# Performance work log

Measured on AMD Instinct MI355X. Metric: run time of the kernel, lower is better.

The kernel has to match this reference:

```python
import jax, jax.numpy as jnp
import numpy as np

WIN = (2, 7, 7)
SHIFT = (1, 3, 3)
HEADS = 4
DIM = 128
MLP_HID = 512
N = WIN[0] * WIN[1] * WIN[2]  # 98
EPS = 1e-5


def _rel_pos_index():
    d = np.arange(WIN[0]); h = np.arange(WIN[1]); w = np.arange(WIN[2])
    coords = np.stack(np.meshgrid(d, h, w, indexing='ij'))  # (3, Wd, Wh, Ww)
    flat = coords.reshape(3, -1)  # (3, N)
    rel = flat[:, :, None] - flat[:, None, :]  # (3, N, N)
    rel = rel.transpose(1, 2, 0).astype(np.int64)  # (N, N, 3)
    rel[..., 0] += WIN[0] - 1
    rel[..., 1] += WIN[1] - 1
    rel[..., 2] += WIN[2] - 1
    rel[..., 0] *= (2 * WIN[1] - 1) * (2 * WIN[2] - 1)
    rel[..., 1] *= (2 * WIN[2] - 1)
    return rel.sum(-1)  # (N, N)


def setup_inputs() -> dict:
    key = jax.random.key(0)
    ks = jax.random.split(key, 8)
    B, D, H, W, C = 4, 8, 56, 56, DIM
    tbl_size = (2 * WIN[0] - 1) * (2 * WIN[1] - 1) * (2 * WIN[2] - 1)  # 507
    s = 0.02
    return {
        'x': jax.random.normal(ks[0], (B, D, H, W, C), jnp.float32),
        'rel_idx': jnp.asarray(_rel_pos_index(), jnp.int32),
        'rpb_table': s * jax.random.normal(ks[1], (tbl_size, HEADS), jnp.float32),
        'qkv_w': s * jax.random.normal(ks[2], (C, 3 * C), jnp.float32),
        'qkv_b': jnp.zeros((3 * C,), jnp.float32),
        'proj_w': s * jax.random.normal(ks[3], (C, C), jnp.float32),
        'proj_b': jnp.zeros((C,), jnp.float32),
        'ln1_g': jnp.ones((C,), jnp.float32),
        'ln1_b': jnp.zeros((C,), jnp.float32),
        'ln2_g': jnp.ones((C,), jnp.float32),
        'ln2_b': jnp.zeros((C,), jnp.float32),
        'mlp_w1': s * jax.random.normal(ks[4], (C, MLP_HID), jnp.float32),
        'mlp_b1': jnp.zeros((MLP_HID,), jnp.float32),
        'mlp_w2': s * jax.random.normal(ks[5], (MLP_HID, C), jnp.float32),
        'mlp_b2': jnp.zeros((C,), jnp.float32),
    }


def _layernorm(x, g, b):
    mu = jnp.mean(x, -1, keepdims=True)
    var = jnp.var(x, -1, keepdims=True)
    return (x - mu) * jax.lax.rsqrt(var + EPS) * g + b


def _window_partition(x):
    B, Dp, Hp, Wp, C = x.shape
    x = x.reshape(B, Dp // WIN[0], WIN[0], Hp // WIN[1], WIN[1], Wp // WIN[2], WIN[2], C)
    x = x.transpose(0, 1, 3, 5, 2, 4, 6, 7)
    return x.reshape(-1, N, C)


def _window_reverse(win, B, Dp, Hp, Wp):
    C = win.shape[-1]
    x = win.reshape(B, Dp // WIN[0], Hp // WIN[1], Wp // WIN[2], WIN[0], WIN[1], WIN[2], C)
    x = x.transpose(0, 1, 4, 2, 5, 3, 6, 7)
    return x.reshape(B, Dp, Hp, Wp, C)


def _block(x, rel_idx, rpb_table, qkv_w, qkv_b, proj_w, proj_b,
           ln1_g, ln1_b, ln2_g, ln2_b, mlp_w1, mlp_b1, mlp_w2, mlp_b2):
    B, D, H, W, C = x.shape
    shortcut = x
    x = _layernorm(x, ln1_g, ln1_b)
    pad_d = (-D) % WIN[0]; pad_h = (-H) % WIN[1]; pad_w = (-W) % WIN[2]
    x = jnp.pad(x, ((0, 0), (0, pad_d), (0, pad_h), (0, pad_w), (0, 0)))
    _, Dp, Hp, Wp, _ = x.shape
    x = jnp.roll(x, (-SHIFT[0], -SHIFT[1], -SHIFT[2]), axis=(1, 2, 3))
    xw = _window_partition(x)  # (B_, N, C)
    B_ = xw.shape[0]
    hd = C // HEADS
    qkv = (xw @ qkv_w + qkv_b).reshape(B_, N, 3, HEADS, hd).transpose(2, 0, 3, 1, 4)
    q, k, v = qkv[0], qkv[1], qkv[2]  # (B_, h, N, hd)
    q = q * (hd ** -0.5)
    attn = jnp.einsum('bhnd,bhmd->bhnm', q, k)
    bias = rpb_table[rel_idx.reshape(-1)].reshape(N, N, HEADS).transpose(2, 0, 1)
    attn = attn + bias[None]
    # NOTE: the original module calls attn with mask=None even when shifted.
    attn = jax.nn.softmax(attn, axis=-1)
    out = jnp.einsum('bhnm,bhmd->bhnd', attn, v).transpose(0, 2, 1, 3).reshape(B_, N, C)
    out = out @ proj_w + proj_b
    x = _window_reverse(out, B, Dp, Hp, Wp)
    x = jnp.roll(x, (SHIFT[0], SHIFT[1], SHIFT[2]), axis=(1, 2, 3))
    x = x[:, :D, :H, :W, :]
    x = shortcut + x
    h1 = _layernorm(x, ln2_g, ln2_b)
    h1 = jax.nn.gelu(h1 @ mlp_w1 + mlp_b1, approximate=False)
    return x + (h1 @ mlp_w2 + mlp_b2)


def reference(x, rel_idx, rpb_table, qkv_w, qkv_b, proj_w, proj_b,
              ln1_g, ln1_b, ln2_g, ln2_b, mlp_w1, mlp_b1, mlp_w2, mlp_b2):
    return _block(x, rel_idx, rpb_table, qkv_w, qkv_b, proj_w, proj_b,
                  ln1_g, ln1_b, ln2_g, ln2_b, mlp_w1, mlp_b1, mlp_w2, mlp_b2)
```

## Files before the change

kernel.cpp:

```cpp
#include <hip/hip_runtime.h>
#include <hip/hip_bf16.h>
#include <cstdint>

#define NWIN   1024
#define NTOK   98
#define BIAS_N 9604

typedef __attribute__((ext_vector_type(8))) short bf16x8;
typedef __attribute__((ext_vector_type(4))) float f32x4;

__device__ __forceinline__ float b2f(unsigned short u) {
  union { uint32_t i; float f; } v; v.i = ((uint32_t)u) << 16; return v.f;
}
__device__ __forceinline__ float b2f_lo(uint32_t u) {
  union { uint32_t i; float f; } v; v.i = u << 16; return v.f;
}
__device__ __forceinline__ float b2f_hi(uint32_t u) {
  union { uint32_t i; float f; } v; v.i = u & 0xffff0000u; return v.f;
}
__device__ __forceinline__ unsigned short f2b(float f) {
  union { float f; uint32_t i; } v; v.f = f;
  uint32_t r = v.i + 0x7fffu + ((v.i >> 16) & 1u);
  return (unsigned short)(r >> 16);
}
__device__ __forceinline__ float ldf(const void* p, size_t i, int f32) {
  return f32 ? ((const float*)p)[i] : b2f(((const unsigned short*)p)[i]);
}
__device__ __forceinline__ float2 ldf2(const void* p, size_t i, int f32) {
  if (f32) { const float* q = (const float*)p + i; return make_float2(q[0], q[1]); }
  uint32_t u = *(const uint32_t*)((const unsigned short*)p + i);
  return make_float2(b2f_lo(u), b2f_hi(u));
}
__device__ __forceinline__ int detect_f32(const uint32_t* __restrict__ xw, int lane) {
  uint32_t w = xw[lane];
  int e = (w >> 23) & 0xFF;
  unsigned long long m = __ballot(e >= 112 && e <= 134);
  return __popcll(m) >= 32;
}
__device__ __forceinline__ float gelu_f(float x) {
  float a = fabsf(x) * 0.70710678118654752f;
  float t = __builtin_amdgcn_rcpf(1.0f + 0.3275911f * a);
  float p = ((((1.061405429f * t - 1.453152027f) * t + 1.421413741f) * t
              - 0.284496736f) * t + 0.254829592f) * t;
  float erfp = 1.0f - p * __expf(-a * a);
  return 0.5f * x * (1.0f + copysignf(erfp, x));
}

#define QG_OFF   0
#define KG_OFF   25690112
#define VGT_OFF  51380224
#define ZPAD_OFF 80740352
#define BIAS_OFF 80748544
#define WQ_OFF   80902208
#define WP_OFF   81000512
#define W1_OFF   81033280
#define W2_OFF   81164352
#define PAR_OFF  81295424
#define FLAG_OFF 81302080
#define LNG_OFF  81302144
#define P_LN1G 0
#define P_LN1B 128
#define P_LN2G 256
#define P_LN2B 384
#define P_QKVB 512
#define P_PROJB 896
#define P_B1  1024
#define P_B2  1536

__global__ __launch_bounds__(256) void prep_kernel(
    const uint32_t* __restrict__ xw,
    const void* __restrict__ qkvw, const void* __restrict__ projw,
    const void* __restrict__ w1, const void* __restrict__ w2,
    const void* __restrict__ ln1g, const void* __restrict__ ln1b,
    const void* __restrict__ ln2g, const void* __restrict__ ln2b,
    const void* __restrict__ qkvb, const void* __restrict__ projb,
    const void* __restrict__ b1, const void* __restrict__ b2,
    const int* __restrict__ rel_idx, const void* __restrict__ tbl,
    unsigned short* __restrict__ wq_t, unsigned short* __restrict__ wp_t,
    unsigned short* __restrict__ w1_t, unsigned short* __restrict__ w2_t,
    float* __restrict__ par, unsigned short* __restrict__ zpad,
    float* __restrict__ bias) {
  const int f32 = detect_f32(xw, threadIdx.x & 63);
  const int bid = blockIdx.x;
  if (bid < 791) {
    int idx = bid * 256 + threadIdx.x;
    if (idx < 49152) {
      int n = idx >> 7, k = idx & 127;
      wq_t[idx] = f2b(ldf(qkvw, (size_t)k * 384 + n, f32));
    } else if ((idx -= 49152) < 16384) {
      int n = idx >> 7, k = idx & 127;
      wp_t[idx] = f2b(ldf(projw, (size_t)k * 128 + n, f32));
    } else if ((idx -= 16384) < 65536) {
      int n = idx >> 7, k = idx & 127;
      w1_t[idx] = f2b(ldf(w1, (size_t)k * 512 + n, f32));
    } else if ((idx -= 65536) < 65536) {
      int n = idx >> 9, k = idx & 511;
      w2_t[idx] = f2b(ldf(w2, (size_t)k * 128 + n, f32));
    } else if ((idx -= 65536) < 1664) {
      float v;
      if      (idx < 128)  v = ldf(ln1g, idx, f32);
      else if (idx < 256)  v = ldf(ln1b, idx - 128, f32);
      else if (idx < 384)  v = ldf(ln2g, idx - 256, f32);
      else if (idx < 512)  v = ldf(ln2b, idx - 384, f32);
      else if (idx < 896)  v = ldf(qkvb, idx - 512, f32);
      else if (idx < 1024) v = ldf(projb, idx - 896, f32);
      else if (idx < 1536) v = ldf(b1, idx - 1024, f32);
      else                 v = ldf(b2, idx - 1536, f32);
      par[idx] = v;
    } else if ((idx -= 1664) < 4096) {
      zpad[idx] = 0;
    }
  } else {
    int i = (bid - 791) * 256 + threadIdx.x;
    if (i < 4 * BIAS_N) {
      int h = i / BIAS_N, ij = i % BIAS_N;
      bias[i] = ldf(tbl, (size_t)rel_idx[ij] * 4 + h, f32);
    }
  }
}

__global__ __launch_bounds__(256, 3) void attn_fused_kernel(
    const void* __restrict__ x,
    const unsigned short* __restrict__ wq_t, const float* __restrict__ bias,
    const unsigned short* __restrict__ wp_t, const float* __restrict__ par,
    unsigned short* __restrict__ kg, unsigned short* __restrict__ vgt,
    unsigned short* __restrict__ lng, void* __restrict__ out) {
  __shared__ __align__(16) unsigned short smem[25872];
  const int f32 = detect_f32((const uint32_t*)x, threadIdx.x & 63);
  const int tid = threadIdx.x, wave = tid >> 6, lane = tid & 63;
  const int quad = lane >> 4, lcol = lane & 15;
  const int win = blockIdx.x, h = wave;
  const int bb = win >> 8, rW = win & 255;
  const int wd = rW >> 6, r2 = rW & 63, wh = r2 >> 3, ww = r2 & 7;

  unsigned short* lnx = smem;
  unsigned short* qs  = smem + 13328;

  for (int t = wave; t < NTOK; t += 4) {
    int td = t / 49, r3 = t % 49, th = r3 / 7, tw = r3 % 7;
    int sd = (wd * 2 + td + 1) & 7;
    int sh = (wh * 7 + th + 3) % 56;
    int sw = (ww * 7 + tw + 3) % 56;
    size_t src = ((((size_t)bb * 8 + sd) * 56 + sh) * 56 + sw) * 128;
    int c0 = lane * 2;
    float2 f = ldf2(x, src + c0, f32);
    float s = f.x + f.y, ss = f.x * f.x + f.y * f.y;
#pragma unroll
    for (int off = 32; off >= 1; off >>= 1) { s += __shfl_xor(s, off); ss += __shfl_xor(ss, off); }
    float mu = s * (1.0f / 128.0f);
    float var = ss * (1.0f / 128.0f) - mu * mu;
    float rs = rsqrtf(var + 1e-5f);
    float y0 = (f.x - mu) * rs * par[P_LN1G + c0] + par[P_LN1B + c0];
    float y1 = (f.y - mu) * rs * par[P_LN1G + c0 + 1] + par[P_LN1B + c0 + 1];
    *(uint32_t*)(lnx + t * 136 + c0) = (uint32_t)f2b(y0) | ((uint32_t)f2b(y1) << 16);
  }
  __syncthreads();

  for (int p = 0; p < 6; ++p) {
    const int n = p * 64 + wave * 16 + lcol;
    bf16x8 bfr[4];
#pragma unroll
    for (int ks4 = 0; ks4 < 4; ++ks4)
      bfr[ks4] = *(const bf16x8*)(wq_t + (size_t)n * 128 + ks4 * 32 + quad * 8);
    const int region = p >> 1;
    const int head = (p & 1) * 2 + (wave >> 1);
    const int d = (wave & 1) * 16 + lcol;
    const float bc = par[P_QKVB + n];
    if (region == 0) {
      unsigned short* dstl = qs + head * 3136 + d;
      for (int mt = 0; mt < 7; ++mt) {
        f32x4 acc = (f32x4){0.f, 0.f, 0.f, 0.f};
#pragma unroll
        for (int ks4 = 0; ks4 < 4; ++ks4) {
          bf16x8 a = *(const bf16x8*)(lnx + min(mt * 16 + lcol, NTOK - 1) * 136 +
                                      ks4 * 32 + quad * 8);
          acc = __builtin_amdgcn_mfma_f32_16x16x32_bf16(a, bfr[ks4], acc, 0, 0, 0);
        }
#pragma unroll
        for (int rr = 0; rr < 4; ++rr) {
          int m = mt * 16 + quad * 4 + rr;
          if (m < NTOK) dstl[m * 32] = f2b((acc[rr] + bc) * 0.17677669529663687f);
        }
      }
    } else if (region == 1) {
      unsigned short* dstg = kg + ((size_t)win * 4 + head) * 3136 + d;
      for (int mt = 0; mt < 7; ++mt) {
        f32x4 acc = (f32x4){0.f, 0.f, 0.f, 0.f};
#pragma unroll
        for (int ks4 = 0; ks4 < 4; ++ks4) {
          bf16x8 a = *(const bf16x8*)(lnx + min(mt * 16 + lcol, NTOK - 1) * 136 +
                                      ks4 * 32 + quad * 8);
          acc = __builtin_amdgcn_mfma_f32_16x16x32_bf16(a, bfr[ks4], acc, 0, 0, 0);
        }
#pragma unroll
        for (int rr = 0; rr < 4; ++rr) {
          int m = mt * 16 + quad * 4 + rr;
          if (m < NTOK) dstg[m * 32] = f2b(acc[rr] + bc);
        }
      }
    } else {
      unsigned short* dstv = vgt + (((size_t)win * 4 + head) * 32 + d) * 112;
      for (int mt = 0; mt < 7; ++mt) {
        f32x4 acc = (f32x4){0.f, 0.f, 0.f, 0.f};
#pragma unroll
        for (int ks4 = 0; ks4 < 4; ++ks4) {
          bf16x8 a = *(const bf16x8*)(lnx + min(mt * 16 + lcol, NTOK - 1) * 136 +
                                      ks4 * 32 + quad * 8);
          acc = __builtin_amdgcn_mfma_f32_16x16x32_bf16(a, bfr[ks4], acc, 0, 0, 0);
        }
        ushort4 w;
        int m0 = mt * 16 + quad * 4;
        w.x = (m0 + 0 < NTOK) ? f2b(acc[0] + bc) : (unsigned short)0;
        w.y = (m0 + 1 < NTOK) ? f2b(acc[1] + bc) : (unsigned short)0;
        w.z = (m0 + 2 < NTOK) ? f2b(acc[2] + bc) : (unsigned short)0;
        w.w = (m0 + 3 < NTOK) ? f2b(acc[3] + bc) : (unsigned short)0;
        *(ushort4*)(dstv + m0) = w;
      }
    }
  }
  __syncthreads();

  const size_t hb = ((size_t)win * 4 + h) * 3136;
  const unsigned short* vbase = vgt + (((size_t)win * 4 + h) * 32) * 112;
  unsigned short* plh = smem + h * 2112;

  bf16x8 aq[7], bk[7];
#pragma unroll
  for (int t = 0; t < 7; ++t) {
    int row = min(t * 16 + lcol, NTOK - 1);
    aq[t] = *(const bf16x8*)(qs + h * 3136 + row * 32 + quad * 8);
    bk[t] = *(const bf16x8*)(kg + hb + (size_t)row * 32 + quad * 8);
  }
  for (int idx = lane; idx < 16 * 16; idx += 64) {
    int rr = idx >> 4, c = 112 + (idx & 15);
    plh[rr * 132 + c] = 0;
  }

  const float* bh = bias + h * BIAS_N;
  f32x4 o[7][2];
  for (int mt = 0; mt < 7; ++mt) {
    f32x4 s[7];
#pragma unroll
    for (int nt = 0; nt < 7; ++nt)
      s[nt] = __builtin_amdgcn_mfma_f32_16x16x32_bf16(aq[mt], bk[nt],
                                                      (f32x4){0.f, 0.f, 0.f, 0.f}, 0, 0, 0);
    const int ib = mt * 16 + quad * 4;
#pragma unroll
    for (int nt = 0; nt < 7; ++nt) {
      int j = nt * 16 + lcol;
      bool jv = j < NTOK;
#pragma unroll
      for (int r = 0; r < 4; ++r) {
        int ic = min(ib + r, NTOK - 1);
        s[nt][r] = jv ? (s[nt][r] + bh[ic * NTOK + j]) : -3.0e38f;
      }
    }
    float mx[4], sum[4], inv[4];
#pragma unroll
    for (int r = 0; r < 4; ++r) {
      float m = s[0][r];
#pragma unroll
      for (int nt = 1; nt < 7; ++nt) m = fmaxf(m, s[nt][r]);
      mx[r] = m;
    }
#pragma unroll
    for (int off = 1; off < 16; off <<= 1)
#pragma unroll
      for (int r = 0; r < 4; ++r) mx[r] = fmaxf(mx[r], __shfl_xor(mx[r], off));
#pragma unroll
    for (int r = 0; r < 4; ++r) sum[r] = 0.f;
#pragma unroll
    for (int nt = 0; nt < 7; ++nt)
#pragma unroll
      for (int r = 0; r < 4; ++r) {
        float e = __expf(s[nt][r] - mx[r]);
        s[nt][r] = e; sum[r] += e;
      }
#pragma unroll
    for (int off = 1; off < 16; off <<= 1)
#pragma unroll
      for (int r = 0; r < 4; ++r) sum[r] += __shfl_xor(sum[r], off);
#pragma unroll
    for (int r = 0; r < 4; ++r) inv[r] = 1.0f / sum[r];
#pragma unroll
    for (int nt = 0; nt < 7; ++nt)
#pragma unroll
      for (int r = 0; r < 4; ++r)
        plh[(quad * 4 + r) * 132 + nt * 16 + lcol] = f2b(s[nt][r] * inv[r]);
#pragma unroll
    for (int n2 = 0; n2 < 2; ++n2) {
      f32x4 acc = (f32x4){0.f, 0.f, 0.f, 0.f};
#pragma unroll
      for (int kp = 0; kp < 4; ++kp) {
        bf16x8 a = *(const bf16x8*)(plh + lcol * 132 + kp * 32 + quad * 8);
        bf16x8 b = *(const bf16x8*)(vbase + (size_t)(n2 * 16 + lcol) * 112 +
                                    kp * 32 + quad * 8);
        acc = __builtin_amdgcn_mfma_f32_16x16x32_bf16(a, b, acc, 0, 0, 0);
      }
      o[mt][n2] = acc;
    }
  }
  __syncthreads();

  unsigned short* olds = smem;
#pragma unroll
  for (int mt = 0; mt < 7; ++mt)
#pragma unroll
    for (int n2 = 0; n2 < 2; ++n2)
#pragma unroll
      for (int r = 0; r < 4; ++r)
        olds[(mt * 16 + quad * 4 + r) * 136 + h * 32 + n2 * 16 + lcol] = f2b(o[mt][n2][r]);
  __syncthreads();

  f32x4 pr[2][7];
  for (int t2 = 0; t2 < 2; ++t2) {
    const int n = (h * 2 + t2) * 16 + lcol;
    bf16x8 bw[4];
#pragma unroll
    for (int kp = 0; kp < 4; ++kp)
      bw[kp] = *(const bf16x8*)(wp_t + (size_t)n * 128 + kp * 32 + quad * 8);
    for (int mt = 0; mt < 7; ++mt) {
      f32x4 acc = (f32x4){0.f, 0.f, 0.f, 0.f};
#pragma unroll
      for (int kp = 0; kp < 4; ++kp) {
        bf16x8 a = *(const bf16x8*)(olds + (mt * 16 + lcol) * 136 + kp * 32 + quad * 8);
        acc = __builtin_amdgcn_mfma_f32_16x16x32_bf16(a, bw[kp], acc, 0, 0, 0);
      }
      pr[t2][mt] = acc;
    }
  }
  __syncthreads();

  const int c = (tid & 31) * 4;
  const float4 gv = *(const float4*)(par + P_LN2G + c);
  const float4 bv = *(const float4*)(par + P_LN2B + c);
  float* pout = (float*)smem;
  for (int pass = 0; pass < 2; ++pass) {
    const int mlo = pass * 56;
    for (int t2 = 0; t2 < 2; ++t2) {
      const int n = (h * 2 + t2) * 16 + lcol;
      const float bc = par[P_PROJB + n];
#pragma unroll
      for (int mt = 0; mt < 7; ++mt)
#pragma unroll
        for (int r = 0; r < 4; ++r) {
          int m = mt * 16 + quad * 4 + r;
          if (m >= mlo && m < mlo + 56 && m < NTOK)
            pout[(m - mlo) * 132 + n] = pr[t2][mt][r] + bc;
        }
    }
    __syncthreads();
    for (int i = tid >> 5; i < 56; i += 8) {
      int m = mlo + i;
      if (m >= NTOK) break;
      int td = m / 49, r3 = m % 49, th = r3 / 7, tw = r3 % 7;
      int sd = (wd * 2 + td + 1) & 7;
      int sh = (wh * 7 + th + 3) % 56;
      int sw = (ww * 7 + tw + 3) % 56;
      size_t base = ((((size_t)bb * 8 + sd) * 56 + sh) * 56 + sw) * 128 + c;
      float4 p = *(const float4*)(pout + i * 132 + c);
      float4 v;
      if (f32) {
        const float4 xr = *(const float4*)((const float*)x + base);
        v = make_float4(p.x + xr.x, p.y + xr.y, p.z + xr.z, p.w + xr.w);
        *(float4*)((float*)out + base) = v;
      } else {
        const ushort4 xr = *(const ushort4*)((const unsigned short*)x + base);
        v = make_float4(p.x + b2f(xr.x), p.y + b2f(xr.y),
                        p.z + b2f(xr.z), p.w + b2f(xr.w));
        ushort4 ov;
        ov.x = f2b(v.x); ov.y = f2b(v.y); ov.z = f2b(v.z); ov.w = f2b(v.w);
        *(ushort4*)((unsigned short*)out + base) = ov;
      }
      float s = v.x + v.y + v.z + v.w;
      float ss = v.x * v.x + v.y * v.y + v.z * v.z + v.w * v.w;
#pragma unroll
      for (int off = 1; off < 32; off <<= 1) {
        s += __shfl_xor(s, off); ss += __shfl_xor(ss, off);
      }
      float mu = s * (1.0f / 128.0f);
      float var = ss * (1.0f / 128.0f) - mu * mu;
      float rs = rsqrtf(var + 1e-5f);
      ushort4 lv;
      lv.x = f2b((v.x - mu) * rs * gv.x + bv.x);
      lv.y = f2b((v.y - mu) * rs * gv.y + bv.y);
      lv.z = f2b((v.z - mu) * rs * gv.z + bv.z);
      lv.w = f2b((v.w - mu) * rs * gv.w + bv.w);
      *(ushort4*)(lng + base) = lv;
    }
    if (pass == 0) __syncthreads();
  }
}

__global__ __launch_bounds__(256) void mlp_kernel(
    const unsigned short* __restrict__ w1_t, const unsigned short* __restrict__ w2_t,
    const float* __restrict__ par, const void* __restrict__ x,
    const unsigned short* __restrict__ lng, void* __restrict__ out) {
  __shared__ __align__(16) unsigned short hbuf[64 * 264];
  const int f32 = detect_f32((const uint32_t*)x, threadIdx.x & 63);
  const int tid = threadIdx.x, wave = tid >> 6, lane = tid & 63;
  const int quad = lane >> 4, lcol = lane & 15;
  const int m0 = blockIdx.x * 64;
  const int nb = wave * 16 + lcol;

  bf16x8 a1[4][4];
#pragma unroll
  for (int mt = 0; mt < 4; ++mt)
#pragma unroll
    for (int ks = 0; ks < 4; ++ks)
      a1[mt][ks] = *(const bf16x8*)(lng + (size_t)(m0 + mt * 16 + lcol) * 128 +
                                    ks * 32 + quad * 8);

  f32x4 acc2[2][4];
#pragma unroll
  for (int a = 0; a < 2; ++a)
#pragma unroll
    for (int b = 0; b < 4; ++b) acc2[a][b] = (f32x4){0.f, 0.f, 0.f, 0.f};

#pragma unroll 1
  for (int g = 0; g < 2; ++g) {
    for (int p = 0; p < 4; ++p) {
      const int nl = p * 64 + nb;
      const int n = g * 256 + nl;
      bf16x8 bfr[4];
#pragma unroll
      for (int ks = 0; ks < 4; ++ks)
        bfr[ks] = *(const bf16x8*)(w1_t + (size_t)n * 128 + ks * 32 + quad * 8);
      const float bc = par[P_B1 + n];
#pragma unroll
      for (int mt = 0; mt < 4; ++mt) {
        f32x4 acc = (f32x4){0.f, 0.f, 0.f, 0.f};
#pragma unroll
        for (int ks = 0; ks < 4; ++ks)
          acc = __builtin_amdgcn_mfma_f32_16x16x32_bf16(a1[mt][ks], bfr[ks], acc, 0, 0, 0);
#pragma unroll
        for (int rr = 0; rr < 4; ++rr) {
          int m = mt * 16 + quad * 4 + rr;
          hbuf[m * 264 + nl] = f2b(gelu_f(acc[rr] + bc));
        }
      }
    }
    __syncthreads();

#pragma unroll
    for (int np = 0; np < 2; ++np) {
      for (int kp = 0; kp < 2; ++kp) {
        bf16x8 b2r[4];
#pragma unroll
        for (int ks = 0; ks < 4; ++ks)
          b2r[ks] = *(const bf16x8*)(w2_t + (size_t)(np * 64 + nb) * 512 + g * 256 +
                                     kp * 128 + ks * 32 + quad * 8);
#pragma unroll
        for (int mt = 0; mt < 4; ++mt) {
#pragma unroll
          for (int ks = 0; ks < 4; ++ks) {
            bf16x8 a = *(const bf16x8*)(hbuf + (mt * 16 + lcol) * 264 + kp * 128 +
                                        ks * 32 + quad * 8);
            acc2[np][mt] = __builtin_amdgcn_mfma_f32_16x16x32_bf16(a, b2r[ks], acc2[np][mt], 0, 0, 0);
          }
        }
      }
    }
    __syncthreads();
  }

  float* pout = (float*)hbuf;
#pragma unroll
  for (int np = 0; np < 2; ++np) {
    const int n = np * 64 + nb;
    const float bc = par[P_B2 + n];
#pragma unroll
    for (int mt = 0; mt < 4; ++mt)
#pragma unroll
      for (int rr = 0; rr < 4; ++rr)
        pout[(mt * 16 + quad * 4 + rr) * 132 + n] = acc2[np][mt][rr] + bc;
  }
  __syncthreads();

  for (int i = tid; i < 2048; i += 256) {
    int t = i >> 5, c = (i & 31) * 4;
    size_t base = (size_t)(m0 + t) * 128 + c;
    float4 p = *(const float4*)(pout + t * 132 + c);
    if (f32) {
      const float4 xr = *(const float4*)((const float*)out + base);
      float4 ov = make_float4(p.x + xr.x, p.y + xr.y, p.z + xr.z, p.w + xr.w);
      *(float4*)((float*)out + base) = ov;
    } else {
      const ushort4 xr = *(const ushort4*)((const unsigned short*)out + base);
      ushort4 ov;
      ov.x = f2b(p.x + b2f(xr.x)); ov.y = f2b(p.y + b2f(xr.y));
      ov.z = f2b(p.z + b2f(xr.z)); ov.w = f2b(p.w + b2f(xr.w));
      *(ushort4*)((unsigned short*)out + base) = ov;
    }
  }
}

extern "C" void kernel_launch(void* const* d_in, const int* in_sizes, int n_in,
                              void* d_out, int out_size, void* d_ws, size_t ws_size,
                              hipStream_t stream) {
  const void* x      = d_in[0];
  const int*  rel    = (const int*)d_in[1];
  const void* rpb    = d_in[2];
  const void* qkv_w  = d_in[3];
  const void* qkv_b  = d_in[4];
  const void* proj_w = d_in[5];
  const void* proj_b = d_in[6];
  const void* ln1_g  = d_in[7];
  const void* ln1_b  = d_in[8];
  const void* ln2_g  = d_in[9];
  const void* ln2_b  = d_in[10];
  const void* w1     = d_in[11];
  const void* b1     = d_in[12];
  const void* w2     = d_in[13];
  const void* b2     = d_in[14];

  char* ws = (char*)d_ws;
  unsigned short* kg   = (unsigned short*)(ws + KG_OFF);
  unsigned short* vgt  = (unsigned short*)(ws + VGT_OFF);
  unsigned short* zpad = (unsigned short*)(ws + ZPAD_OFF);
  float*          bias = (float*)(ws + BIAS_OFF);
  unsigned short* wq_t = (unsigned short*)(ws + WQ_OFF);
  unsigned short* wp_t = (unsigned short*)(ws + WP_OFF);
  unsigned short* w1_t = (unsigned short*)(ws + W1_OFF);
  unsigned short* w2_t = (unsigned short*)(ws + W2_OFF);
  float*          par  = (float*)(ws + PAR_OFF);
  unsigned short* lng  = (unsigned short*)(ws + LNG_OFF);

  prep_kernel<<<791 + 151, 256, 0, stream>>>(
      (const uint32_t*)x, qkv_w, proj_w, w1, w2, ln1_g, ln1_b, ln2_g, ln2_b,
      qkv_b, proj_b, b1, b2, rel, rpb,
      wq_t, wp_t, w1_t, w2_t, par, zpad, bias);
  attn_fused_kernel<<<NWIN, 256, 0, stream>>>(x, wq_t, bias, wp_t, par,
                                              kg, vgt, lng, d_out);
  mlp_kernel<<<100352 / 64, 256, 0, stream>>>(w1_t, w2_t, par, x, lng, d_out);
}
```

Baseline: 364.0 us.

## Transpose and pad bias table, give each wave its own head's QKV, drop barrier

The relative-position bias is now precomputed transposed and zero-padded to 112x112 per head, so each lane loads four consecutive bias values with one float4 load instead of four scalar gathers. The QKV projection is remapped so each wave computes the Q, K and V columns of its own head. That removes the block-wide barrier between the projection and attention phases, leaving only a per-wave wait on outstanding memory ops. The P scratch buffer now reuses that wave's own Q region in shared memory instead of a separate slice. The risk is correctness: any later phase that still assumes cross-wave visibility could race, and the larger bias table adds prep work.

After: 363.3 us. About the same (-0.2%).

```diff
diff --git a/kernel.cpp b/kernel.cpp
--- a/kernel.cpp
+++ b/kernel.cpp
@@ -46,17 +46,15 @@
   return 0.5f * x * (1.0f + copysignf(erfp, x));
 }
 
-#define QG_OFF   0
+#define BIAST_OFF 0
 #define KG_OFF   25690112
 #define VGT_OFF  51380224
 #define ZPAD_OFF 80740352
-#define BIAS_OFF 80748544
 #define WQ_OFF   80902208
 #define WP_OFF   81000512
 #define W1_OFF   81033280
 #define W2_OFF   81164352
 #define PAR_OFF  81295424
-#define FLAG_OFF 81302080
 #define LNG_OFF  81302144
 #define P_LN1G 0
 #define P_LN1B 128
@@ -79,7 +77,7 @@
     unsigned short* __restrict__ wq_t, unsigned short* __restrict__ wp_t,
     unsigned short* __restrict__ w1_t, unsigned short* __restrict__ w2_t,
     float* __restrict__ par, unsigned short* __restrict__ zpad,
-    float* __restrict__ bias) {
+    float* __restrict__ bias_t) {
   const int f32 = detect_f32(xw, threadIdx.x & 63);
   const int bid = blockIdx.x;
   if (bid < 791) {
@@ -111,17 +109,19 @@
       zpad[idx] = 0;
     }
   } else {
-    int i = (bid - 791) * 256 + threadIdx.x;
-    if (i < 4 * BIAS_N) {
-      int h = i / BIAS_N, ij = i % BIAS_N;
-      bias[i] = ldf(tbl, (size_t)rel_idx[ij] * 4 + h, f32);
+    int t = (bid - 791) * 256 + threadIdx.x;
+    if (t < 4 * 112 * 112) {
+      int h = t / 12544, rem = t % 12544, j = rem / 112, i = rem % 112;
+      float v = 0.f;
+      if (i < NTOK && j < NTOK) v = ldf(tbl, (size_t)rel_idx[i * NTOK + j] * 4 + h, f32);
+      bias_t[t] = v;
     }
   }
 }
 
 __global__ __launch_bounds__(256, 3) void attn_fused_kernel(
     const void* __restrict__ x,
-    const unsigned short* __restrict__ wq_t, const float* __restrict__ bias,
+    const unsigned short* __restrict__ wq_t, const float* __restrict__ bias_t,
     const unsigned short* __restrict__ wp_t, const float* __restrict__ par,
     unsigned short* __restrict__ kg, unsigned short* __restrict__ vgt,
     unsigned short* __restrict__ lng, void* __restrict__ out) {
@@ -157,17 +157,16 @@
   __syncthreads();
 
   for (int p = 0; p < 6; ++p) {
-    const int n = p * 64 + wave * 16 + lcol;
+    const int region = p >> 1;
+    const int d = (p & 1) * 16 + lcol;
+    const int n = region * 128 + h * 32 + d;
     bf16x8 bfr[4];
 #pragma unroll
     for (int ks4 = 0; ks4 < 4; ++ks4)
       bfr[ks4] = *(const bf16x8*)(wq_t + (size_t)n * 128 + ks4 * 32 + quad * 8);
-    const int region = p >> 1;
-    const int head = (p & 1) * 2 + (wave >> 1);
-    const int d = (wave & 1) * 16 + lcol;
     const float bc = par[P_QKVB + n];
     if (region == 0) {
-      unsigned short* dstl = qs + head * 3136 + d;
+      unsigned short* dstl = qs + h * 3136 + d;
       for (int mt = 0; mt < 7; ++mt) {
         f32x4 acc = (f32x4){0.f, 0.f, 0.f, 0.f};
 #pragma unroll
@@ -183,7 +182,7 @@
         }
       }
     } else if (region == 1) {
-      unsigned short* dstg = kg + ((size_t)win * 4 + head) * 3136 + d;
+      unsigned short* dstg = kg + ((size_t)win * 4 + h) * 3136 + d;
       for (int mt = 0; mt < 7; ++mt) {
         f32x4 acc = (f32x4){0.f, 0.f, 0.f, 0.f};
 #pragma unroll
@@ -199,7 +198,7 @@
         }
       }
     } else {
-      unsigned short* dstv = vgt + (((size_t)win * 4 + head) * 32 + d) * 112;
+      unsigned short* dstv = vgt + (((size_t)win * 4 + h) * 32 + d) * 112;
       for (int mt = 0; mt < 7; ++mt) {
         f32x4 acc = (f32x4){0.f, 0.f, 0.f, 0.f};
 #pragma unroll
@@ -218,11 +217,10 @@
       }
     }
   }
-  __syncthreads();
+  asm volatile("s_waitcnt vmcnt(0)" ::: "memory");
 
   const size_t hb = ((size_t)win * 4 + h) * 3136;
   const unsigned short* vbase = vgt + (((size_t)win * 4 + h) * 32) * 112;
-  unsigned short* plh = smem + h * 2112;
 
   bf16x8 aq[7], bk[7];
 #pragma unroll
@@ -231,12 +229,13 @@
     aq[t] = *(const bf16x8*)(qs + h * 3136 + row * 32 + quad * 8);
     bk[t] = *(const bf16x8*)(kg + hb + (size_t)row * 32 + quad * 8);
   }
+  unsigned short* plh = qs + h * 3136;
   for (int idx = lane; idx < 16 * 16; idx += 64) {
     int rr = idx >> 4, c = 112 + (idx & 15);
     plh[rr * 132 + c] = 0;
   }
 
-  const float* bh = bias + h * BIAS_N;
+  const float* bh = bias_t + h * 12544;
   f32x4 o[7][2];
   for (int mt = 0; mt < 7; ++mt) {
     f32x4 s[7];
@@ -249,11 +248,11 @@
     for (int nt = 0; nt < 7; ++nt) {
       int j = nt * 16 + lcol;
       bool jv = j < NTOK;
-#pragma unroll
-      for (int r = 0; r < 4; ++r) {
-        int ic = min(ib + r, NTOK - 1);
-        s[nt][r] = jv ? (s[nt][r] + bh[ic * NTOK + j]) : -3.0e38f;
-      }
+      const float4 bv4 = *(const float4*)(bh + j * 112 + ib);
+      s[nt][0] = jv ? (s[nt][0] + bv4.x) : -3.0e38f;
+      s[nt][1] = jv ? (s[nt][1] + bv4.y) : -3.0e38f;
+      s[nt][2] = jv ? (s[nt][2] + bv4.z) : -3.0e38f;
+      s[nt][3] = jv ? (s[nt][3] + bv4.w) : -3.0e38f;
     }
     float mx[4], sum[4], inv[4];
 #pragma unroll
@@ -515,10 +514,10 @@
   const void* b2     = d_in[14];
 
   char* ws = (char*)d_ws;
+  float*          bias_t = (float*)(ws + BIAST_OFF);
   unsigned short* kg   = (unsigned short*)(ws + KG_OFF);
   unsigned short* vgt  = (unsigned short*)(ws + VGT_OFF);
   unsigned short* zpad = (unsigned short*)(ws + ZPAD_OFF);
-  float*          bias = (float*)(ws + BIAS_OFF);
   unsigned short* wq_t = (unsigned short*)(ws + WQ_OFF);
   unsigned short* wp_t = (unsigned short*)(ws + WP_OFF);
   unsigned short* w1_t = (unsigned short*)(ws + W1_OFF);
@@ -526,11 +525,11 @@
   float*          par  = (float*)(ws + PAR_OFF);
   unsigned short* lng  = (unsigned short*)(ws + LNG_OFF);
 
-  prep_kernel<<<791 + 151, 256, 0, stream>>>(
+  prep_kernel<<<791 + 196, 256, 0, stream>>>(
       (const uint32_t*)x, qkv_w, proj_w, w1, w2, ln1_g, ln1_b, ln2_g, ln2_b,
       qkv_b, proj_b, b1, b2, rel, rpb,
-      wq_t, wp_t, w1_t, w2_t, par, zpad, bias);
-  attn_fused_kernel<<<NWIN, 256, 0, stream>>>(x, wq_t, bias, wp_t, par,
+      wq_t, wp_t, w1_t, w2_t, par, zpad, bias_t);
+  attn_fused_kernel<<<NWIN, 256, 0, stream>>>(x, wq_t, bias_t, wp_t, par,
                                               kg, vgt, lng, d_out);
   mlp_kernel<<<100352 / 64, 256, 0, stream>>>(w1_t, w2_t, par, x, lng, d_out);
 }
```
